# Optimization experiments

Measured on AMD Instinct MI355X. Metric: run time of the kernel, lower is better.

Reference implementation:

```python
import jax, jax.numpy as jnp
import numpy as np

N_NODES = 50000
N_EDGES = 400000
N_GRAPHS = 256
HID = 128
FEAT_IN, POS_IN, EDGE_IN = 64, 16, 16
N_LAYERS = 4


def _lin(x, w, b):
    return x @ w.T + b


def setup_inputs() -> dict:
    key = jax.random.key(0)
    ks = iter(jax.random.split(key, 64))
    s = 0.05

    def w(shape):
        return (jax.random.normal(next(ks), shape, dtype=jnp.float32) * s)

    inp = {
        "h": jax.random.normal(next(ks), (N_NODES, FEAT_IN), dtype=jnp.float32),
        "e": jax.random.normal(next(ks), (N_EDGES, EDGE_IN), dtype=jnp.float32),
        "p": jax.random.normal(next(ks), (N_NODES, POS_IN), dtype=jnp.float32),
        "edge_index": jax.random.randint(next(ks), (2, N_EDGES), 0, N_NODES),
        "batch": jnp.sort(jax.random.randint(next(ks), (N_NODES,), 0, N_GRAPHS)),
        # embeddings
        "h_embed_w": w((HID, FEAT_IN)), "h_embed_b": w((HID,)),
        "e_embed_w": w((HID, EDGE_IN)), "e_embed_b": w((HID,)),
        "p_embed_w": w((HID, POS_IN)), "p_embed_b": w((HID,)),
        # per-layer params, stacked over layers
        "hu_w": w((N_LAYERS, HID, 5 * HID)), "hu_b": w((N_LAYERS, HID)),
        "eu_w": w((N_LAYERS, HID, 3 * HID)), "eu_b": w((N_LAYERS, HID)),
        "pu_w": w((N_LAYERS, HID, 3 * HID)), "pu_b": w((N_LAYERS, HID)),
        "hagg_w": w((N_LAYERS, HID, 2 * HID)), "hagg_b": w((N_LAYERS, HID)),
        "pagg_w": w((N_LAYERS, HID, 2 * HID)), "pagg_b": w((N_LAYERS, HID)),
        # readout MLP
        "r1_w": w((HID, 2 * HID)), "r1_b": w((HID,)),
        "r2_w": w((HID // 2, HID)), "r2_b": w((HID // 2,)),
        "r3_w": w((1, HID // 2)), "r3_b": w((1,)),
    }
    return inp


def reference(h, e, p, edge_index, batch,
              h_embed_w, h_embed_b, e_embed_w, e_embed_b, p_embed_w, p_embed_b,
              hu_w, hu_b, eu_w, eu_b, pu_w, pu_b,
              hagg_w, hagg_b, pagg_w, pagg_b,
              r1_w, r1_b, r2_w, r2_b, r3_w, r3_b):
    send, rec = edge_index[0], edge_index[1]
    N = h.shape[0]

    h = _lin(h, h_embed_w, h_embed_b)
    e = _lin(e, e_embed_w, e_embed_b)
    p = _lin(p, p_embed_w, p_embed_b)

    for l in range(N_LAYERS):
        hp_send = jnp.concatenate((h[send], p[send]), axis=1)  # [E, 2H]
        hp_rec = jnp.concatenate((h[rec], p[rec]), axis=1)     # [E, 2H]
        h_msg = _lin(jnp.concatenate((hp_send, hp_rec, e), axis=1), hu_w[l], hu_b[l])
        h_msg_agg = jax.ops.segment_sum(h_msg, rec, num_segments=N)
        h = _lin(jnp.concatenate((h, h_msg_agg), axis=1), hagg_w[l], hagg_b[l])
        e = _lin(jnp.concatenate((h[send], h[rec], e), axis=1), eu_w[l], eu_b[l])
        p_msg = _lin(jnp.concatenate((p[send], p[rec], e), axis=1), pu_w[l], pu_b[l])
        p_msg_agg = jax.ops.segment_sum(p_msg, rec, num_segments=N)
        p = _lin(jnp.concatenate((p, p_msg_agg), axis=1), pagg_w[l], pagg_b[l])

    h_agg = jax.ops.segment_sum(h, batch, num_segments=N_GRAPHS)
    p_agg = jax.ops.segment_sum(p, batch, num_segments=N_GRAPHS)
    hep = jnp.concatenate((h_agg, p_agg), axis=1)
    x = jax.nn.relu(_lin(hep, r1_w, r1_b))
    x = jax.nn.relu(_lin(x, r2_w, r2_b))
    out = _lin(x, r3_w, r3_b).squeeze(-1)  # [N_GRAPHS]
    return (out, p)
```

## Files before the change

kernel.cpp:

```cpp
#include <hip/hip_runtime.h>

typedef __attribute__((ext_vector_type(8))) short bf16x8;
typedef __attribute__((ext_vector_type(4))) float f32x4;
typedef __attribute__((ext_vector_type(4))) unsigned short us4;

__device__ __forceinline__ float b2f(unsigned short h) {
  union { unsigned int u; float f; } v; v.u = ((unsigned int)h) << 16; return v.f;
}
__device__ __forceinline__ unsigned short f2b(float f) {
  union { float f; unsigned int u; } v; v.f = f;
  unsigned int r = v.u + 0x7fffu + ((v.u >> 16) & 1u);
  return (unsigned short)(r >> 16);
}

__device__ __forceinline__ bf16x8 scale8(bf16x8 a, float d) {
  bf16x8 r;
#pragma unroll
  for (int i = 0; i < 8; ++i) {
    union { unsigned int u; float f; } v;
    v.u = ((unsigned int)(unsigned short)a[i]) << 16;
    r[i] = (short)f2b(v.f * d);
  }
  return r;
}

__global__ void f2b_kernel(const float* __restrict__ in, unsigned short* __restrict__ out, int n4) {
  int i = blockIdx.x * blockDim.x + threadIdx.x;
  int stride = gridDim.x * blockDim.x;
  for (; i < n4; i += stride) {
    float4 v = reinterpret_cast<const float4*>(in)[i];
    us4 o;
    o[0] = f2b(v.x); o[1] = f2b(v.y); o[2] = f2b(v.z); o[3] = f2b(v.w);
    reinterpret_cast<us4*>(out)[i] = o;
  }
}

__launch_bounds__(256)
__global__ void compose_w(const float* __restrict__ hg, const float* __restrict__ hu,
                          const float* __restrict__ pg, const float* __restrict__ pu,
                          const float* __restrict__ hub, const float* __restrict__ pub,
                          unsigned short* __restrict__ wh, unsigned short* __restrict__ wp,
                          float* __restrict__ bh, float* __restrict__ bp) {
  __shared__ float As[128][129];
  __shared__ float Bs[128][36];
  __shared__ float bvs[128];
  const int l = blockIdx.x >> 5, t = blockIdx.x & 31;
  const float* A; const float* B; const float* bv; unsigned short* W; float* bo;
  int lda, ldb, ldw, cbase, wbase, dbase;
  if (t < 20) {
    A = hg + (size_t)l * 128 * 256; lda = 256;
    B = hu + (size_t)l * 128 * 640; ldb = 640;
    W = wh + (size_t)l * 128 * 768; ldw = 768;
    bv = hub + l * 128; bo = bh + l * 128; cbase = t * 32;
    wbase = (cbase < 256) ? cbase : (cbase < 512 ? cbase + 256 : cbase - 256);
    dbase = 384;
  } else {
    A = pg + (size_t)l * 128 * 256; lda = 256;
    B = pu + (size_t)l * 128 * 384; ldb = 384;
    W = wp + (size_t)l * 128 * 512; ldw = 512;
    bv = pub + l * 128; bo = bp + l * 128; cbase = (t - 20) * 32;
    wbase = (cbase < 128) ? cbase : (cbase < 256 ? cbase + 256 : cbase - 128);
    dbase = 256;
  }
  const int tid = threadIdx.x;
  for (int idx = tid; idx < 128 * 128; idx += 256) {
    int r = idx >> 7, c = idx & 127;
    As[r][c] = A[r * lda + 128 + c];
  }
  for (int idx = tid; idx < 128 * 32; idx += 256) {
    int m = idx >> 5, c = idx & 31;
    Bs[m][c] = B[m * ldb + cbase + c];
  }
  if (tid < 128) bvs[tid] = bv[tid];
  __syncthreads();
  const int o = tid & 127, g = tid >> 7;
  float acc[16];
#pragma unroll
  for (int j = 0; j < 16; ++j) acc[j] = 0.f;
  for (int m = 0; m < 128; ++m) {
    float a = As[o][m];
#pragma unroll
    for (int j4 = 0; j4 < 4; ++j4) {
      float4 b4 = *reinterpret_cast<const float4*>(&Bs[m][g * 16 + j4 * 4]);
      acc[j4 * 4 + 0] += a * b4.x; acc[j4 * 4 + 1] += a * b4.y;
      acc[j4 * 4 + 2] += a * b4.z; acc[j4 * 4 + 3] += a * b4.w;
    }
  }
#pragma unroll
  for (int j4 = 0; j4 < 4; ++j4) {
    us4 ov;
    ov[0] = f2b(acc[j4 * 4 + 0]); ov[1] = f2b(acc[j4 * 4 + 1]);
    ov[2] = f2b(acc[j4 * 4 + 2]); ov[3] = f2b(acc[j4 * 4 + 3]);
    *reinterpret_cast<us4*>(&W[(long)o * ldw + wbase + g * 16 + j4 * 4]) = ov;
  }
  if (cbase == 0) {
    for (int idx = tid; idx < 128 * 128; idx += 256) {
      int oo = idx >> 7, m = idx & 127;
      W[(long)oo * ldw + dbase + m] = f2b(A[oo * lda + m]);
    }
    if (tid < 128) {
      float s = 0.f;
      for (int m = 0; m < 128; ++m) s += As[tid][m] * bvs[m];
      bo[tid] = s;
    }
  }
}

__launch_bounds__(256, 3)
__global__ void embed_mfma64(const unsigned short* __restrict__ xb, const unsigned short* __restrict__ w64,
                             const float* __restrict__ b, unsigned short* __restrict__ out, int M) {
  __shared__ __align__(16) unsigned short ldsW[2 * 8 * 64 * 8];
  const int tid = threadIdx.x;
  const int wid = tid >> 6, lane = tid & 63;
  const long rowBase = (long)blockIdx.x * 128 + wid * 32;
  const int lq = lane >> 4;
  const int lr = lane & 15;

#pragma unroll
  for (int it = 0; it < 4; ++it) {
    int f = tid + it * 256;
    int sub = f >> 9, r = f & 511;
    int t = r >> 6, l = r & 63;
    int n = t * 16 + (l & 15);
    int kk = sub * 32 + ((l >> 4) * 8);
    *reinterpret_cast<bf16x8*>(&ldsW[f * 8]) =
        *reinterpret_cast<const bf16x8*>(&w64[(long)n * 64 + kk]);
  }
  __syncthreads();

  int rowD[2];
#pragma unroll
  for (int am = 0; am < 2; ++am) {
    long e = rowBase + am * 16 + lr;
    if (e >= M) e = M - 1;
    rowD[am] = (int)e;
  }

  f32x4 acc[2][8];
#pragma unroll
  for (int i = 0; i < 2; ++i)
#pragma unroll
    for (int j = 0; j < 8; ++j) acc[i][j] = 0.f;

#pragma unroll
  for (int s = 0; s < 2; ++s) {
    bf16x8 a[2];
#pragma unroll
    for (int am = 0; am < 2; ++am)
      a[am] = *reinterpret_cast<const bf16x8*>(&xb[(long)rowD[am] * 64 + s * 32 + lq * 8]);
#pragma unroll
    for (int n = 0; n < 8; ++n) {
      bf16x8 bb = *reinterpret_cast<const bf16x8*>(&ldsW[((s << 9) + (n << 6) + lane) * 8]);
      acc[0][n] = __builtin_amdgcn_mfma_f32_16x16x32_bf16(a[0], bb, acc[0][n], 0, 0, 0);
      acc[1][n] = __builtin_amdgcn_mfma_f32_16x16x32_bf16(a[1], bb, acc[1][n], 0, 0, 0);
    }
  }

  float bo[8];
#pragma unroll
  for (int n = 0; n < 8; ++n) bo[n] = b[n * 16 + lr];

#pragma unroll
  for (int am = 0; am < 2; ++am) {
#pragma unroll
    for (int r = 0; r < 4; ++r) {
      long row = rowBase + am * 16 + lq * 4 + r;
      if (row < M) {
#pragma unroll
        for (int n = 0; n < 8; ++n)
          out[row * 256 + n * 16 + lr] = f2b(acc[am][n][r] + bo[n]);
      }
    }
  }
}

template<int K>
__launch_bounds__(256)
__global__ void embed_fast(const float* __restrict__ in, const float* __restrict__ w,
                           const float* __restrict__ b, unsigned short* __restrict__ out,
                           long M, int ostride, int ocoloff, const float* __restrict__ degB) {
  __shared__ float wT[K][129];
  __shared__ float xt[16 * K];
  const int tid = threadIdx.x;
  const int col = tid & 127;
  const int half = tid >> 7;
  for (int idx = tid; idx < 128 * K; idx += 256) {
    int c = idx / K, k = idx % K;
    wT[k][c] = w[idx];
  }
  __syncthreads();
  float wreg[K];
#pragma unroll
  for (int k = 0; k < K; ++k) wreg[k] = wT[k][col];
  const float bcol = b[col];

  for (long r0 = (long)blockIdx.x * 16; r0 < M; r0 += (long)gridDim.x * 16) {
    __syncthreads();
    const float4* src4 = reinterpret_cast<const float4*>(in + r0 * K);
    const int n4 = 16 * K / 4;
    if (r0 + 16 <= M) {
      for (int i = tid; i < n4; i += 256)
        reinterpret_cast<float4*>(xt)[i] = src4[i];
    } else {
      int rem = (int)((M - r0) * K) / 4;
      for (int i = tid; i < n4; i += 256) {
        float4 z = {0.f, 0.f, 0.f, 0.f};
        reinterpret_cast<float4*>(xt)[i] = (i < rem) ? src4[i] : z;
      }
    }
    __syncthreads();
#pragma unroll
    for (int rr = 0; rr < 8; ++rr) {
      long row = r0 + half * 8 + rr;
      if (row >= M) break;
      const float* xr = &xt[(half * 8 + rr) * K];
      float acc = bcol * (degB ? degB[row] : 1.0f);
#pragma unroll
      for (int k4 = 0; k4 < K / 4; ++k4) {
        float4 xv = reinterpret_cast<const float4*>(xr)[k4];
        acc += xv.x * wreg[k4 * 4] + xv.y * wreg[k4 * 4 + 1] +
               xv.z * wreg[k4 * 4 + 2] + xv.w * wreg[k4 * 4 + 3];
      }
      out[row * ostride + ocoloff + col] = f2b(acc);
    }
  }
}

__global__ void count_deg(const int* __restrict__ rec, int* __restrict__ deg, int E) {
  int i = blockIdx.x * blockDim.x + threadIdx.x;
  if (i < E) atomicAdd(&deg[rec[i]], 1);
}

__global__ void scan_blk(const int* __restrict__ deg, int* __restrict__ tmp,
                         int* __restrict__ blkSum, int N) {
  __shared__ int ts[256];
  const int b = blockIdx.x, t = threadIdx.x;
  const int base = b * 1024 + t * 4;
  int v0 = (base + 0 < N) ? deg[base + 0] : 0;
  int v1 = (base + 1 < N) ? deg[base + 1] : 0;
  int v2 = (base + 2 < N) ? deg[base + 2] : 0;
  int v3 = (base + 3 < N) ? deg[base + 3] : 0;
  int tsum = v0 + v1 + v2 + v3;
  ts[t] = tsum;
  __syncthreads();
  for (int off = 1; off < 256; off <<= 1) {
    int x = (t >= off) ? ts[t - off] : 0;
    __syncthreads();
    ts[t] += x;
    __syncthreads();
  }
  int texcl = ts[t] - tsum;
  if (base + 0 < N) tmp[base + 0] = texcl;
  if (base + 1 < N) tmp[base + 1] = texcl + v0;
  if (base + 2 < N) tmp[base + 2] = texcl + v0 + v1;
  if (base + 3 < N) tmp[base + 3] = texcl + v0 + v1 + v2;
  if (t == 255) blkSum[b] = ts[255];
}

__global__ void scan_top(int* __restrict__ blkSum, int nb) {
  __shared__ int s[64];
  int t = threadIdx.x;
  if (t < nb) s[t] = blkSum[t];
  __syncthreads();
  if (t == 0) {
    int run = 0;
    for (int i = 0; i < nb; ++i) { int x = s[i]; s[i] = run; run += x; }
  }
  __syncthreads();
  if (t < nb) blkSum[t] = s[t];
}

__global__ void scan_fix(const int* __restrict__ deg, int* __restrict__ row_ptr,
                         const int* __restrict__ blkOff, int* __restrict__ cursor,
                         float* __restrict__ degF, int N, int E) {
  const int b = blockIdx.x, t = threadIdx.x;
  const int base = b * 1024 + t * 4;
  const int off = blkOff[b];
#pragma unroll
  for (int k = 0; k < 4; ++k) {
    int i = base + k;
    if (i < N) {
      int v = row_ptr[i] + off;
      row_ptr[i] = v;
      cursor[i] = v;
      degF[i] = (float)deg[i];
    }
  }
  if (b == 0 && t == 0) row_ptr[N] = E;
}

__global__ void scatter_perm(const int* __restrict__ rec, const int* __restrict__ send,
                             int* __restrict__ cursor, int* __restrict__ perm,
                             int* __restrict__ sendP, int E) {
  int i = blockIdx.x * blockDim.x + threadIdx.x;
  if (i < E) {
    int pos = atomicAdd(&cursor[rec[i]], 1);
    perm[pos] = i;
    sendP[pos] = send[i];
  }
}

__global__ void segsum_raw(const float* __restrict__ eraw, const int* __restrict__ row_ptr,
                           const int* __restrict__ perm, float* __restrict__ out16, int N) {
  int sub = threadIdx.x >> 4;
  int f = threadIdx.x & 15;
  int r = blockIdx.x * 16 + sub;
  if (r >= N) return;
  int j0 = row_ptr[r], j1 = row_ptr[r + 1];
  float s0 = 0.f, s1 = 0.f;
  int j = j0;
  for (; j + 2 <= j1; j += 2) {
    int e0 = perm[j], e1 = perm[j + 1];
    s0 += eraw[(long)e0 * 16 + f];
    s1 += eraw[(long)e1 * 16 + f];
  }
  if (j < j1) s0 += eraw[(long)perm[j] * 16 + f];
  out16[(long)r * 16 + f] = s0 + s1;
}

__launch_bounds__(256)
__global__ void gather_sum256(const unsigned short* __restrict__ src,
                              const int* __restrict__ row_ptr, const int* __restrict__ sendP,
                              unsigned short* __restrict__ dst, int N) {
  const int wid = threadIdx.x >> 6, lane = threadIdx.x & 63;
  const int r = blockIdx.x * 4 + wid;
  if (r >= N) return;
  const int j0 = row_ptr[r], j1 = row_ptr[r + 1];
  const int off = lane * 4;
  float a0 = 0.f, a1 = 0.f, a2 = 0.f, a3 = 0.f;
  int j = j0;
  for (; j + 4 <= j1; j += 4) {
    int i0 = sendP[j], i1 = sendP[j + 1], i2 = sendP[j + 2], i3 = sendP[j + 3];
    us4 x = *reinterpret_cast<const us4*>(&src[(long)i0 * 256 + off]);
    us4 y = *reinterpret_cast<const us4*>(&src[(long)i1 * 256 + off]);
    us4 z = *reinterpret_cast<const us4*>(&src[(long)i2 * 256 + off]);
    us4 w = *reinterpret_cast<const us4*>(&src[(long)i3 * 256 + off]);
    a0 += b2f(x[0]) + b2f(y[0]) + b2f(z[0]) + b2f(w[0]);
    a1 += b2f(x[1]) + b2f(y[1]) + b2f(z[1]) + b2f(w[1]);
    a2 += b2f(x[2]) + b2f(y[2]) + b2f(z[2]) + b2f(w[2]);
    a3 += b2f(x[3]) + b2f(y[3]) + b2f(z[3]) + b2f(w[3]);
  }
  for (; j < j1; ++j) {
    us4 x = *reinterpret_cast<const us4*>(&src[(long)sendP[j] * 256 + off]);
    a0 += b2f(x[0]); a1 += b2f(x[1]); a2 += b2f(x[2]); a3 += b2f(x[3]);
  }
  us4 o;
  o[0] = f2b(a0); o[1] = f2b(a1); o[2] = f2b(a2); o[3] = f2b(a3);
  *reinterpret_cast<us4*>(&dst[(long)r * 256 + off]) = o;
}

__launch_bounds__(256)
__global__ void gather_sum128(const unsigned short* __restrict__ src, int col,
                              const int* __restrict__ row_ptr, const int* __restrict__ sendP,
                              unsigned short* __restrict__ dst, int N) {
  const int wid = threadIdx.x >> 6, lane = threadIdx.x & 63;
  const int r = blockIdx.x * 4 + wid;
  if (r >= N) return;
  const int j0 = row_ptr[r], j1 = row_ptr[r + 1];
  const int half = lane >> 5;
  const int c = lane & 31;
  const int off = col + c * 4;
  float a0 = 0.f, a1 = 0.f, a2 = 0.f, a3 = 0.f;
  float b0 = 0.f, b1 = 0.f, b2 = 0.f, b3 = 0.f;
  int j = j0 + half;
  for (; j + 6 < j1; j += 8) {
    int i0 = sendP[j], i1 = sendP[j + 2], i2 = sendP[j + 4], i3 = sendP[j + 6];
    us4 x = *reinterpret_cast<const us4*>(&src[(long)i0 * 256 + off]);
    us4 y = *reinterpret_cast<const us4*>(&src[(long)i1 * 256 + off]);
    us4 z = *reinterpret_cast<const us4*>(&src[(long)i2 * 256 + off]);
    us4 w = *reinterpret_cast<const us4*>(&src[(long)i3 * 256 + off]);
    a0 += b2f(x[0]) + b2f(z[0]); a1 += b2f(x[1]) + b2f(z[1]);
    a2 += b2f(x[2]) + b2f(z[2]); a3 += b2f(x[3]) + b2f(z[3]);
    b0 += b2f(y[0]) + b2f(w[0]); b1 += b2f(y[1]) + b2f(w[1]);
    b2 += b2f(y[2]) + b2f(w[2]); b3 += b2f(y[3]) + b2f(w[3]);
  }
  for (; j + 2 < j1; j += 4) {
    int i0 = sendP[j], i1 = sendP[j + 2];
    us4 x = *reinterpret_cast<const us4*>(&src[(long)i0 * 256 + off]);
    us4 y = *reinterpret_cast<const us4*>(&src[(long)i1 * 256 + off]);
    a0 += b2f(x[0]); a1 += b2f(x[1]); a2 += b2f(x[2]); a3 += b2f(x[3]);
    b0 += b2f(y[0]); b1 += b2f(y[1]); b2 += b2f(y[2]); b3 += b2f(y[3]);
  }
  if (j < j1) {
    us4 x = *reinterpret_cast<const us4*>(&src[(long)sendP[j] * 256 + off]);
    a0 += b2f(x[0]); a1 += b2f(x[1]); a2 += b2f(x[2]); a3 += b2f(x[3]);
  }
  a0 += b0; a1 += b1; a2 += b2; a3 += b3;
  a0 += __shfl_xor(a0, 32); a1 += __shfl_xor(a1, 32);
  a2 += __shfl_xor(a2, 32); a3 += __shfl_xor(a3, 32);
  if (half == 0) {
    us4 o;
    o[0] = f2b(a0); o[1] = f2b(a1); o[2] = f2b(a2); o[3] = f2b(a3);
    *reinterpret_cast<us4*>(&dst[(long)r * 256 + off]) = o;
  }
}

__launch_bounds__(256, 3)
__global__ void gemm_mp(int M, int nsrc, int Kw, int srcsel, int coloffs, int sflags,
                        const unsigned short* __restrict__ sp0, const unsigned short* __restrict__ sp1,
                        const unsigned short* __restrict__ sp2,
                        const unsigned short* __restrict__ Wb,
                        const float* __restrict__ bdeg, const float* __restrict__ bone,
                        const float* __restrict__ degF,
                        unsigned short* __restrict__ outB, int ostride, int ocoloff,
                        float* __restrict__ outF) {
  __shared__ __align__(16) unsigned short ldsW[2 * 8 * 64 * 8];
  const int tid = threadIdx.x;
  const int wid = tid >> 6, lane = tid & 63;
  const long rowBase = (long)blockIdx.x * 128 + wid * 32;
  const int lq = lane >> 4;
  const int lr = lane & 15;

  int rowD[2];
  float degD[2];
#pragma unroll
  for (int am = 0; am < 2; ++am) {
    long e = rowBase + am * 16 + lr;
    if (e >= M) e = M - 1;
    rowD[am] = (int)e;
    degD[am] = degF[rowD[am]];
  }

  f32x4 acc[2][8];
#pragma unroll
  for (int i = 0; i < 2; ++i)
#pragma unroll
    for (int j = 0; j < 8; ++j) acc[i][j] = 0.f;

  int wcol = 0;
  for (int si = 0; si < nsrc; ++si) {
    const int sel = (srcsel >> (si * 4)) & 15;
    const unsigned short* sp = (sel == 0) ? sp0 : (sel == 1) ? sp1 : sp2;
    const long astride = (sel == 2) ? 128 : 256;
    const int acoloff = ((coloffs >> (si * 4)) & 15) * 128;
    const int f = (sflags >> (si * 4)) & 15;
    const int nrep = (f == 1) ? 2 : 1;
    for (int rep = 0; rep < nrep; ++rep) {
      const bool sc = (f == 2) || (rep == 1);
      const int wbase = wcol + rep * 128;
#pragma unroll 2
      for (int h = 0; h < 2; ++h) {
        bf16x8 a[2][2];
#pragma unroll
        for (int s = 0; s < 2; ++s) {
          const int koff = acoloff + h * 64 + s * 32 + lq * 8;
#pragma unroll
          for (int am = 0; am < 2; ++am)
            a[am][s] = *reinterpret_cast<const bf16x8*>(&sp[(long)rowD[am] * astride + koff]);
        }
        __syncthreads();
#pragma unroll
        for (int it = 0; it < 4; ++it) {
          int fi = tid + it * 256;
          int sub = fi >> 9, r = fi & 511;
          int t = r >> 6, l = r & 63;
          int n = t * 16 + (l & 15);
          int kk = wbase + h * 64 + sub * 32 + ((l >> 4) * 8);
          *reinterpret_cast<bf16x8*>(&ldsW[fi * 8]) =
              *reinterpret_cast<const bf16x8*>(&Wb[(long)n * Kw + kk]);
        }
        __syncthreads();
#pragma unroll
        for (int s = 0; s < 2; ++s) {
          bf16x8 av0 = sc ? scale8(a[0][s], degD[0]) : a[0][s];
          bf16x8 av1 = sc ? scale8(a[1][s], degD[1]) : a[1][s];
#pragma unroll
          for (int n = 0; n < 8; ++n) {
            bf16x8 b = *reinterpret_cast<const bf16x8*>(&ldsW[((s << 9) + (n << 6) + lane) * 8]);
            acc[0][n] = __builtin_amdgcn_mfma_f32_16x16x32_bf16(av0, b, acc[0][n], 0, 0, 0);
            acc[1][n] = __builtin_amdgcn_mfma_f32_16x16x32_bf16(av1, b, acc[1][n], 0, 0, 0);
          }
        }
      }
    }
    wcol += nrep * 128;
  }

  float bd[8], bo[8];
#pragma unroll
  for (int n = 0; n < 8; ++n) {
    bd[n] = bdeg ? bdeg[n * 16 + lr] : 0.f;
    bo[n] = bone ? bone[n * 16 + lr] : 0.f;
  }

#pragma unroll
  for (int am = 0; am < 2; ++am) {
#pragma unroll
    for (int r = 0; r < 4; ++r) {
      long row = rowBase + am * 16 + lq * 4 + r;
      if (row < M) {
        float d = degF[row];
        long ob = row * ostride + ocoloff;
#pragma unroll
        for (int n = 0; n < 8; ++n) {
          float v = acc[am][n][r] + bd[n] * d + bo[n];
          outB[ob + n * 16 + lr] = f2b(v);
          if (outF) outF[row * 128 + n * 16 + lr] = v;
        }
      }
    }
  }
}

__global__ void readout_agg(const unsigned short* __restrict__ hp,
                            const int* __restrict__ batch, float* __restrict__ hep, int N) {
  int col = threadIdx.x;
  int n0 = blockIdx.x * 128;
  int n1 = n0 + 128; if (n1 > N) n1 = N;
  float sum = 0.f; int curg = -1;
  for (int n = n0; n < n1; ++n) {
    int g = batch[n];
    if (g != curg) {
      if (curg >= 0) unsafeAtomicAdd(&hep[(long)curg * 256 + col], sum);
      curg = g; sum = 0.f;
    }
    sum += b2f(hp[(long)n * 256 + col]);
  }
  if (curg >= 0) unsafeAtomicAdd(&hep[(long)curg * 256 + col], sum);
}

__global__ void mlp_kernel(const float* __restrict__ hep,
                           const float* __restrict__ r1w, const float* __restrict__ r1b,
                           const float* __restrict__ r2w, const float* __restrict__ r2b,
                           const float* __restrict__ r3w, const float* __restrict__ r3b,
                           float* __restrict__ out) {
  int g = blockIdx.x, t = threadIdx.x;
  __shared__ float x[256];
  __shared__ float y[128];
  __shared__ float z[64];
  x[t] = hep[(long)g * 256 + t];
  x[t + 128] = hep[(long)g * 256 + 128 + t];
  __syncthreads();
  float s = r1b[t];
  for (int k = 0; k < 256; ++k) s += r1w[t * 256 + k] * x[k];
  y[t] = fmaxf(s, 0.f);
  __syncthreads();
  if (t < 64) {
    float s2 = r2b[t];
    for (int k = 0; k < 128; ++k) s2 += r2w[t * 128 + k] * y[k];
    z[t] = fmaxf(s2, 0.f);
  }
  __syncthreads();
  if (t == 0) {
    float s3 = r3b[0];
    for (int k = 0; k < 64; ++k) s3 += r3w[k] * z[k];
    out[g] = s3;
  }
}

extern "C" void kernel_launch(void* const* d_in, const int* in_sizes, int n_in,
                              void* d_out, int out_size, void* d_ws, size_t ws_size,
                              hipStream_t stream) {
  const float* h_in = (const float*)d_in[0];
  const float* e_in = (const float*)d_in[1];
  const float* p_in = (const float*)d_in[2];
  const int* ei = (const int*)d_in[3];
  const int* batch = (const int*)d_in[4];
  const float* he_w = (const float*)d_in[5];  const float* he_b = (const float*)d_in[6];
  const float* ee_w = (const float*)d_in[7];  const float* ee_b = (const float*)d_in[8];
  const float* pe_w = (const float*)d_in[9];  const float* pe_b = (const float*)d_in[10];
  const float* hu_w = (const float*)d_in[11]; const float* hu_b = (const float*)d_in[12];
  const float* eu_w = (const float*)d_in[13]; const float* eu_b = (const float*)d_in[14];
  const float* pu_w = (const float*)d_in[15]; const float* pu_b = (const float*)d_in[16];
  const float* hg_w = (const float*)d_in[17]; const float* hg_b = (const float*)d_in[18];
  const float* pg_w = (const float*)d_in[19]; const float* pg_b = (const float*)d_in[20];
  const float* r1w = (const float*)d_in[21];  const float* r1b = (const float*)d_in[22];
  const float* r2w = (const float*)d_in[23];  const float* r2b = (const float*)d_in[24];
  const float* r3w = (const float*)d_in[25];  const float* r3b = (const float*)d_in[26];

  const int N = 50000, E = 400000, G = 256;
  const int* send = ei;
  const int* rec = ei + E;

  char* ws = (char*)d_ws;
  size_t off = 0;
  auto alloc = [&](size_t bytes) {
    void* pp = ws + off;
    off += (bytes + 255) & ~(size_t)255;
    return pp;
  };
  unsigned short* hp  = (unsigned short*)alloc((size_t)N * 256 * 2);
  unsigned short* gHP = (unsigned short*)alloc((size_t)N * 256 * 2);
  unsigned short* sT  = (unsigned short*)alloc((size_t)N * 128 * 2);
  unsigned short* hb16 = (unsigned short*)alloc((size_t)N * 64 * 2);
  unsigned short* w_he = (unsigned short*)alloc((size_t)128 * 64 * 2);
  float* segsumF = (float*)alloc((size_t)N * 16 * 4);
  int* deg = (int*)alloc((size_t)N * 4);
  int* row_ptr = (int*)alloc((size_t)(N + 1) * 4);
  int* cursor = (int*)alloc((size_t)N * 4);
  int* blkSum = (int*)alloc((size_t)64 * 4);
  int* perm = (int*)alloc((size_t)E * 4);
  int* sendP = (int*)alloc((size_t)E * 4);
  float* degF = (float*)alloc((size_t)N * 4);
  float* hep = (float*)alloc((size_t)G * 256 * 4);
  unsigned short* w_h2 = (unsigned short*)alloc((size_t)4 * 128 * 768 * 2);
  unsigned short* w_p2 = (unsigned short*)alloc((size_t)4 * 128 * 512 * 2);
  unsigned short* w_eu = (unsigned short*)alloc((size_t)4 * 128 * 384 * 2);
  float* bh1 = (float*)alloc((size_t)4 * 128 * 4);
  float* bp1 = (float*)alloc((size_t)4 * 128 * 4);
  (void)ws_size; (void)n_in; (void)in_sizes; (void)out_size;

  f2b_kernel<<<192, 256, 0, stream>>>(eu_w, w_eu, 4 * 128 * 384 / 4);
  f2b_kernel<<<2048, 256, 0, stream>>>(h_in, hb16, N * 64 / 4);
  f2b_kernel<<<8, 256, 0, stream>>>(he_w, w_he, 128 * 64 / 4);
  compose_w<<<128, 256, 0, stream>>>(hg_w, hu_w, pg_w, pu_w, hu_b, pu_b, w_h2, w_p2, bh1, bp1);

  const int nb = (N + 1023) / 1024;
  hipMemsetAsync(deg, 0, (size_t)N * 4, stream);
  count_deg<<<(E + 255) / 256, 256, 0, stream>>>(rec, deg, E);
  scan_blk<<<nb, 256, 0, stream>>>(deg, row_ptr, blkSum, N);
  scan_top<<<1, 64, 0, stream>>>(blkSum, nb);
  scan_fix<<<nb, 256, 0, stream>>>(deg, row_ptr, blkSum, cursor, degF, N, E);
  scatter_perm<<<(E + 255) / 256, 256, 0, stream>>>(rec, send, cursor, perm, sendP, E);

  embed_mfma64<<<(N + 127) / 128, 256, 0, stream>>>(hb16, w_he, he_b, hp, N);
  embed_fast<16><<<3125, 256, 0, stream>>>(p_in, pe_w, pe_b, hp, N, 256, 128, nullptr);
  segsum_raw<<<(N + 15) / 16, 256, 0, stream>>>(e_in, row_ptr, perm, segsumF, N);
  embed_fast<16><<<3125, 256, 0, stream>>>(segsumF, ee_w, ee_b, sT, N, 128, 0, degF);

  gather_sum256<<<(N + 3) / 4, 256, 0, stream>>>(hp, row_ptr, sendP, gHP, N);

  float* pOut = (float*)d_out + 256;
  const int gridN = (N + 127) / 128;
  const int gridG = (N + 3) / 4;

  for (int l = 0; l < 4; ++l) {
    gemm_mp<<<gridN, 256, 0, stream>>>(N, 5, 768, 0x11200, 0x10010, 0x21000,
        gHP, hp, sT,
        w_h2 + (size_t)l * 128 * 768, bh1 + l * 128, hg_b + l * 128, degF,
        hp, 256, 0, nullptr);
    gather_sum128<<<gridG, 256, 0, stream>>>(hp, 0, row_ptr, sendP, gHP, N);
    gemm_mp<<<gridN, 256, 0, stream>>>(N, 3, 384, 0x210, 0x000, 0x020,
        gHP, hp, sT,
        w_eu + (size_t)l * 128 * 384, eu_b + l * 128, nullptr, degF,
        sT, 128, 0, nullptr);
    gemm_mp<<<gridN, 256, 0, stream>>>(N, 3, 512, 0x120, 0x101, 0x100,
        gHP, hp, sT,
        w_p2 + (size_t)l * 128 * 512, bp1 + l * 128, pg_b + l * 128, degF,
        hp, 256, 128, (l == 3) ? pOut : nullptr);
    if (l < 3)
      gather_sum128<<<gridG, 256, 0, stream>>>(hp, 128, row_ptr, sendP, gHP, N);
  }

  hipMemsetAsync(hep, 0, (size_t)G * 256 * 4, stream);
  readout_agg<<<(N + 127) / 128, 256, 0, stream>>>(hp, batch, hep, N);
  mlp_kernel<<<G, 128, 0, stream>>>(hep, r1w, r1b, r2w, r2b, r3w, r3b, (float*)d_out);
}
```

Before: 733.8 us.

## Restructure gemm_mp K-loop to reuse A loads across reps with smaller W tiles

Reorders the gemm_mp inner loops so each 32-wide K slice of the activation rows is loaded once and reused for both the plain and degree-scaled weight passes, instead of reloading it per rep. The shared-memory weight tile shrinks from 64 to 32 K columns, halving LDS use per block. In exchange, the number of __syncthreads barriers per K element doubles and less work is done between syncs, which may expose global-load latency.

```diff
diff --git a/kernel.cpp b/kernel.cpp
--- a/kernel.cpp
+++ b/kernel.cpp
@@ -404,7 +404,7 @@
                         const float* __restrict__ degF,
                         unsigned short* __restrict__ outB, int ostride, int ocoloff,
                         float* __restrict__ outF) {
-  __shared__ __align__(16) unsigned short ldsW[2 * 8 * 64 * 8];
+  __shared__ __align__(16) unsigned short ldsW[8 * 64 * 8];
   const int tid = threadIdx.x;
   const int wid = tid >> 6, lane = tid & 63;
   const long rowBase = (long)blockIdx.x * 128 + wid * 32;
@@ -435,41 +435,34 @@
     const int acoloff = ((coloffs >> (si * 4)) & 15) * 128;
     const int f = (sflags >> (si * 4)) & 15;
     const int nrep = (f == 1) ? 2 : 1;
-    for (int rep = 0; rep < nrep; ++rep) {
-      const bool sc = (f == 2) || (rep == 1);
-      const int wbase = wcol + rep * 128;
-#pragma unroll 2
-      for (int h = 0; h < 2; ++h) {
-        bf16x8 a[2][2];
-#pragma unroll
-        for (int s = 0; s < 2; ++s) {
-          const int koff = acoloff + h * 64 + s * 32 + lq * 8;
-#pragma unroll
-          for (int am = 0; am < 2; ++am)
-            a[am][s] = *reinterpret_cast<const bf16x8*>(&sp[(long)rowD[am] * astride + koff]);
-        }
+#pragma unroll 4
+    for (int sub = 0; sub < 4; ++sub) {
+      const int koff = acoloff + sub * 32 + lq * 8;
+      bf16x8 a[2];
+#pragma unroll
+      for (int am = 0; am < 2; ++am)
+        a[am] = *reinterpret_cast<const bf16x8*>(&sp[(long)rowD[am] * astride + koff]);
+      for (int rep = 0; rep < nrep; ++rep) {
+        const bool sc = (f == 2) || (rep == 1);
+        const int wk = wcol + rep * 128 + sub * 32;
         __syncthreads();
 #pragma unroll
-        for (int it = 0; it < 4; ++it) {
-          int fi = tid + it * 256;
-          int sub = fi >> 9, r = fi & 511;
-          int t = r >> 6, l = r & 63;
+        for (int it = 0; it < 2; ++it) {
+          int idx = tid + it * 256;
+          int t = idx >> 6, l = idx & 63;
           int n = t * 16 + (l & 15);
-          int kk = wbase + h * 64 + sub * 32 + ((l >> 4) * 8);
-          *reinterpret_cast<bf16x8*>(&ldsW[fi * 8]) =
+          int kk = wk + ((l >> 4) * 8);
+          *reinterpret_cast<bf16x8*>(&ldsW[idx * 8]) =
               *reinterpret_cast<const bf16x8*>(&Wb[(long)n * Kw + kk]);
         }
         __syncthreads();
-#pragma unroll
-        for (int s = 0; s < 2; ++s) {
-          bf16x8 av0 = sc ? scale8(a[0][s], degD[0]) : a[0][s];
-          bf16x8 av1 = sc ? scale8(a[1][s], degD[1]) : a[1][s];
-#pragma unroll
-          for (int n = 0; n < 8; ++n) {
-            bf16x8 b = *reinterpret_cast<const bf16x8*>(&ldsW[((s << 9) + (n << 6) + lane) * 8]);
-            acc[0][n] = __builtin_amdgcn_mfma_f32_16x16x32_bf16(av0, b, acc[0][n], 0, 0, 0);
-            acc[1][n] = __builtin_amdgcn_mfma_f32_16x16x32_bf16(av1, b, acc[1][n], 0, 0, 0);
-          }
+        bf16x8 av0 = sc ? scale8(a[0], degD[0]) : a[0];
+        bf16x8 av1 = sc ? scale8(a[1], degD[1]) : a[1];
+#pragma unroll
+        for (int n = 0; n < 8; ++n) {
+          bf16x8 b = *reinterpret_cast<const bf16x8*>(&ldsW[(n * 64 + lane) * 8]);
+          acc[0][n] = __builtin_amdgcn_mfma_f32_16x16x32_bf16(av0, b, acc[0][n], 0, 0, 0);
+          acc[1][n] = __builtin_amdgcn_mfma_f32_16x16x32_bf16(av1, b, acc[1][n], 0, 0, 0);
         }
       }
     }
```

New measurement: 703.3 us. -4.2%, faster.
